# Kernel tuning notes

Hardware: AMD Instinct MI355X
Metric: run time of the kernel (lower is better)

Reference implementation:

```python
import jax, jax.numpy as jnp
import numpy as np

B, S, D = 8, 2048, 768

def setup_inputs():
    key = jax.random.key(0)
    k1, k2, k3, k4 = jax.random.split(key, 4)
    hidden = jax.random.normal(k1, (B, S, D), dtype=jnp.float32)
    # relative lengths in [0.5, 1.0) so every sequence has a realistic valid region
    lengths = 0.5 + 0.5 * jax.random.uniform(k2, (B,), dtype=jnp.float32)
    s = 1.0 / np.sqrt(D)
    W1 = jax.random.uniform(k3, (D, D), minval=-s, maxval=s, dtype=jnp.float32)
    b1 = jnp.zeros((D,), jnp.float32)
    W2 = jax.random.uniform(k4, (D,), minval=-s, maxval=s, dtype=jnp.float32)
    b2 = jnp.zeros((), jnp.float32)
    return {"hidden": hidden, "lengths": lengths, "W1": W1, "b1": b1, "W2": W2, "b2": b2}

def _boundaries(hidden, lengths, W1, b1, W2, b2):
    # Eval-mode boundary prediction (dropout = identity, soft = probs).
    Bn, Sn, _ = hidden.shape
    actual_lens = (lengths * Sn).astype(jnp.int32)                      # [B]
    valid = (jnp.arange(Sn)[None, :] < actual_lens[:, None]).astype(hidden.dtype)  # [B,S]
    h = jax.nn.gelu(hidden @ W1 + b1, approximate=False)                # torch nn.GELU is exact
    logits = h @ W2 + b2                                                # [B,S]
    probs = jax.nn.sigmoid(logits)
    soft = probs * valid
    hard = (probs > 0.5).astype(hidden.dtype) * valid
    last_valid = jnp.clip(actual_lens - 1, 0, Sn - 1)
    bi = jnp.arange(Bn)
    soft = soft.at[bi, last_valid].set(1.0)
    hard = hard.at[bi, last_valid].set(1.0)
    hard_b = hard - jax.lax.stop_gradient(soft) + soft                  # straight-through
    return hard_b, probs * valid, valid, actual_lens

def reference(hidden, lengths, W1, b1, W2, b2):
    Bn, Sn, Dn = hidden.shape
    hard_b, masked_probs, valid, actual_lens = _boundaries(hidden, lengths, W1, b1, W2, b2)
    # K = max segments in the batch (data-dependent -> computed eagerly, as
    # the original torch code does with .item() inside common()).
    K = int(jnp.max(jnp.sum(jax.lax.stop_gradient(hard_b), axis=1)))
    # segment id of each position: boundary token ENDS its segment
    seg_id = jnp.cumsum(hard_b, axis=1) - hard_b                        # [B,S]
    seg_onehot = (jnp.arange(K)[None, None, :]
                  == jax.lax.stop_gradient(seg_id)[:, :, None])          # [B,S,K] == (foo==0)
    segment_mask = seg_onehot.astype(hidden.dtype) * valid[:, :, None]
    counts = jnp.maximum(segment_mask.sum(axis=1), 1.0)                 # [B,K]
    # dense one-hot mask-matmul segment mean, matching the torch bmm formulation
    pooled = jnp.einsum('bsk,bsd->bkd', segment_mask, hidden) / counts[:, :, None]
    nb = (hard_b * valid).sum(axis=1)                                   # boundaries / sample
    max_segments = max(K, 1)
    full = nb >= max_segments - 1
    partial = (nb > 0) & (nb < max_segments - 1)
    shortened = jnp.where(full, 1.0,
                          jnp.where(partial, (nb + 1.0) / max_segments, 0.0))
    return pooled, masked_probs, shortened, nb, actual_lens.astype(jnp.float32)
```

## Files before the change

### kernel.cpp

```cpp
#include <hip/hip_runtime.h>
#include <math.h>

typedef __bf16 bf16x8 __attribute__((ext_vector_type(8)));
typedef float  f32x4  __attribute__((ext_vector_type(4)));

#define NT2 12

__device__ inline float gelu_f(float x) {
    return 0.5f * x * (1.0f + erff(x * 0.70710678118654752f));
}

typedef const __attribute__((address_space(1))) void* gas_t;
typedef __attribute__((address_space(3))) void*       las_t;
__device__ __forceinline__ void gl_lds16(const void* g, void* l) {
    __builtin_amdgcn_global_load_lds((gas_t)g, (las_t)l, 16, 0, 0);
}

__global__ __launch_bounds__(256) void s0_w1t(
    const float* __restrict__ W1, __bf16* __restrict__ Wt, int Dn)
{
    __shared__ float tile[32][33];
    const int k0 = blockIdx.x * 32;
    const int n0 = blockIdx.y * 32;
    const int tx = threadIdx.x & 31, ty = threadIdx.x >> 5;
    #pragma unroll
    for (int p = 0; p < 4; ++p)
        tile[ty + p * 8][tx] = W1[(size_t)(k0 + ty + p * 8) * Dn + n0 + tx];
    __syncthreads();
    #pragma unroll
    for (int p = 0; p < 4; ++p) {
        const int n = n0 + ty + p * 8, k = k0 + tx;
        Wt[(size_t)n * Dn + k] = (__bf16)tile[tx][ty + p * 8];
    }
}

__global__ __launch_bounds__(512) void k1_hyb(
    const float* __restrict__ X, const __bf16* __restrict__ W1t,
    const float* __restrict__ b1, const float* __restrict__ W2,
    float* __restrict__ partial, int Kd)
{
    __shared__ __bf16 Ash[2][128 * 32];
    __shared__ __bf16 Bsh[2][128 * 32];

    const int t    = threadIdx.x;
    const int lane = t & 63;
    const int w    = t >> 6;
    const int wr   = w >> 1;
    const int wc   = w & 1;
    const int ln15 = lane & 15, lg = lane >> 4;
    const int m0   = blockIdx.x * 128;
    const int n0   = blockIdx.y * 128;

    const int ar  = t >> 2, aq = t & 3;
    const int asw = (ar >> 1) & 3;
    const float* gA = X + (size_t)(m0 + ar) * Kd + aq * 8;
    const int    awr = ar * 32 + (aq ^ asw) * 8;

    const int brow = t >> 2;
    const int bkw  = (t & 3) ^ ((brow >> 1) & 3);
    const __bf16* gB = W1t + (size_t)(n0 + brow) * Kd + bkw * 8;

    int aoff[2], boff[4];
    #pragma unroll
    for (int mf = 0; mf < 2; ++mf) {
        const int r = wr * 32 + mf * 16 + ln15;
        aoff[mf] = r * 32 + (lg ^ ((r >> 1) & 3)) * 8;
    }
    #pragma unroll
    for (int nf = 0; nf < 4; ++nf) {
        const int r = wc * 64 + nf * 16 + ln15;
        boff[nf] = r * 32 + (lg ^ ((r >> 1) & 3)) * 8;
    }

    f32x4 acc[2][4];
    #pragma unroll
    for (int i = 0; i < 2; ++i)
        #pragma unroll
        for (int j = 0; j < 4; ++j)
            acc[i][j] = (f32x4){0.f, 0.f, 0.f, 0.f};

    {
        const float4 lo = *(const float4*)(gA);
        const float4 hi = *(const float4*)(gA + 4);
        bf16x8 ab;
        ab[0] = (__bf16)lo.x; ab[1] = (__bf16)lo.y;
        ab[2] = (__bf16)lo.z; ab[3] = (__bf16)lo.w;
        ab[4] = (__bf16)hi.x; ab[5] = (__bf16)hi.y;
        ab[6] = (__bf16)hi.z; ab[7] = (__bf16)hi.w;
        *(bf16x8*)&Ash[0][awr] = ab;
        gl_lds16(gB, &Bsh[0][t * 8]);
    }
    __syncthreads();

    const int nt = Kd / 32;
    int cur = 0;
    for (int kt = 0; kt < nt; ++kt) {
        float4 alo, ahi;
        const bool more = (kt + 1 < nt);
        if (more) {
            const int ko = (kt + 1) * 32;
            alo = *(const float4*)(gA + ko);
            ahi = *(const float4*)(gA + ko + 4);
            gl_lds16(gB + ko, &Bsh[cur ^ 1][t * 8]);
        }

        bf16x8 fa[2], fb[4];
        #pragma unroll
        for (int mf = 0; mf < 2; ++mf)
            fa[mf] = *(const bf16x8*)&Ash[cur][aoff[mf]];
        #pragma unroll
        for (int nf = 0; nf < 4; ++nf)
            fb[nf] = *(const bf16x8*)&Bsh[cur][boff[nf]];
        #pragma unroll
        for (int mf = 0; mf < 2; ++mf)
            #pragma unroll
            for (int nf = 0; nf < 4; ++nf)
                acc[mf][nf] = __builtin_amdgcn_mfma_f32_16x16x32_bf16(
                    fa[mf], fb[nf], acc[mf][nf], 0, 0, 0);

        if (more) {
            bf16x8 ab;
            ab[0] = (__bf16)alo.x; ab[1] = (__bf16)alo.y;
            ab[2] = (__bf16)alo.z; ab[3] = (__bf16)alo.w;
            ab[4] = (__bf16)ahi.x; ab[5] = (__bf16)ahi.y;
            ab[6] = (__bf16)ahi.z; ab[7] = (__bf16)ahi.w;
            *(bf16x8*)&Ash[cur ^ 1][awr] = ab;
        }
        __syncthreads();
        cur ^= 1;
    }

    float b1v[4], w2v[4];
    #pragma unroll
    for (int nf = 0; nf < 4; ++nf) {
        const int n = n0 + wc * 64 + nf * 16 + ln15;
        b1v[nf] = b1[n];
        w2v[nf] = W2[n];
    }
    #pragma unroll
    for (int mf = 0; mf < 2; ++mf)
        #pragma unroll
        for (int j = 0; j < 4; ++j) {
            float s = 0.f;
            #pragma unroll
            for (int nf = 0; nf < 4; ++nf) {
                float c = acc[mf][nf][j] + b1v[nf];
                s += gelu_f(c) * w2v[nf];
            }
            s += __shfl_xor(s, 1);
            s += __shfl_xor(s, 2);
            s += __shfl_xor(s, 4);
            s += __shfl_xor(s, 8);
            if (ln15 == 0) {
                const int m = m0 + wr * 32 + mf * 16 + lg * 4 + j;
                partial[(size_t)m * NT2 + blockIdx.y * 2 + wc] = s;
            }
        }
}

__global__ __launch_bounds__(256) void k2a_logits(
    const float* __restrict__ partial, const float* __restrict__ lengths,
    const float* __restrict__ b2p, float* __restrict__ logits,
    float* __restrict__ out_probs, int S)
{
    const int idx = blockIdx.x * 256 + threadIdx.x;
    const int b = idx / S, s = idx - b * S;
    float sum = b2p[0];
    #pragma unroll
    for (int jt = 0; jt < NT2; ++jt)
        sum += partial[(size_t)idx * NT2 + jt];
    logits[idx] = sum;
    const int len = (int)(lengths[b] * (float)S);
    out_probs[idx] = (s < len) ? 1.0f / (1.0f + expf(-sum)) : 0.0f;
}

__global__ __launch_bounds__(256) void k2b_scan(
    const float* __restrict__ logits, const float* __restrict__ lengths,
    float* __restrict__ out_short, float* __restrict__ out_nb,
    float* __restrict__ out_lens, int* __restrict__ bpos,
    int* __restrict__ nb_arr, int S, int K)
{
    const int b = blockIdx.x;
    const int t = threadIdx.x;
    const int len = (int)(lengths[b] * (float)S);

    __shared__ int cnt[256];
    __shared__ int flags_s[2048];

    const int RP = S / 256;
    const int base_s = t * RP;
    int local = 0;
    #pragma unroll
    for (int r = 0; r < 8; ++r) {
        int s = base_s + r;
        bool v = (s < len);
        int f = (s == len - 1) ? 1 : ((v && logits[(size_t)b * S + s] > 0.0f) ? 1 : 0);
        flags_s[s] = f;
        local += f;
    }
    cnt[t] = local;
    __syncthreads();
    for (int off = 1; off < 256; off <<= 1) {
        int v = cnt[t];
        int u = (t >= off) ? cnt[t - off] : 0;
        __syncthreads();
        cnt[t] = v + u;
        __syncthreads();
    }
    int excl = cnt[t] - local;
    int total = cnt[255];
    for (int r = 0; r < RP; ++r) {
        int s = base_s + r;
        if (flags_s[s]) { bpos[b * S + excl] = s; ++excl; }
    }
    if (t == 0) {
        nb_arr[b] = total;
        float nbf = (float)total;
        float Kf  = (float)K;
        out_nb[b]   = nbf;
        out_lens[b] = (float)len;
        float sh;
        if (nbf >= Kf - 1.0f)      sh = 1.0f;
        else if (nbf > 0.0f)       sh = (nbf + 1.0f) / Kf;
        else                       sh = 0.0f;
        out_short[b] = sh;
    }
}

__global__ __launch_bounds__(192) void k3_pool(
    const float* __restrict__ X, const int* __restrict__ bpos,
    const int* __restrict__ nb_arr, float* __restrict__ pooled,
    int S, int D, int K)
{
    const int bk = blockIdx.x;
    const int b  = bk / K;
    const int k  = bk - b * K;
    const int t  = threadIdx.x;
    const int nb = nb_arr[b];

    float4 acc = {0.f, 0.f, 0.f, 0.f};
    if (k < nb) {
        int start = (k == 0) ? 0 : (bpos[b * S + k - 1] + 1);
        int end   = bpos[b * S + k] + 1;
        float cntf = (float)(end - start);
        for (int s = start; s < end; ++s) {
            const float4 v = *(const float4*)&X[((size_t)b * S + s) * D + t * 4];
            acc.x += v.x; acc.y += v.y; acc.z += v.z; acc.w += v.w;
        }
        acc.x /= cntf; acc.y /= cntf; acc.z /= cntf; acc.w /= cntf;
    }
    *(float4*)&pooled[((size_t)b * K + k) * D + t * 4] = acc;
}

extern "C" void kernel_launch(void* const* d_in, const int* in_sizes, int n_in,
                              void* d_out, int out_size, void* d_ws, size_t ws_size,
                              hipStream_t stream) {
    const float* hidden  = (const float*)d_in[0];
    const float* lengths = (const float*)d_in[1];
    const float* W1      = (const float*)d_in[2];
    const float* b1      = (const float*)d_in[3];
    const float* W2      = (const float*)d_in[4];
    const float* b2      = (const float*)d_in[5];

    const int B = in_sizes[1];
    const int D = in_sizes[3];
    const int S = in_sizes[0] / (B * D);
    const int M = B * S;
    const int K = (out_size - B * S - 3 * B) / (B * D);

    float* out_pooled = (float*)d_out;
    float* out_probs  = out_pooled + (size_t)B * K * D;
    float* out_short  = out_probs + (size_t)B * S;
    float* out_nb     = out_short + B;
    float* out_lens   = out_nb + B;

    char* wsp = (char*)d_ws;
    float* partial = (float*)wsp; wsp += (size_t)M * NT2 * sizeof(float);
    float* logits  = (float*)wsp; wsp += (size_t)M * sizeof(float);
    int*   bpos    = (int*)wsp;   wsp += (size_t)M * sizeof(int);
    int*   nb_arr  = (int*)wsp;

    __bf16* W1t = (__bf16*)out_pooled;

    dim3 gs(D / 32, D / 32);
    s0_w1t<<<gs, 256, 0, stream>>>(W1, W1t, D);

    dim3 g1(M / 128, D / 128);
    k1_hyb<<<g1, 512, 0, stream>>>(hidden, W1t, b1, W2, partial, D);

    k2a_logits<<<M / 256, 256, 0, stream>>>(partial, lengths, b2, logits,
                                            out_probs, S);
    k2b_scan<<<B, 256, 0, stream>>>(logits, lengths, out_short, out_nb,
                                    out_lens, bpos, nb_arr, S, K);
    k3_pool<<<B * K, D / 4, 0, stream>>>(hidden, bpos, nb_arr, out_pooled, S, D, K);
}
```

Measured before the change: 59.11 us.

## Widen GEMM tile to 128x256 with 2x4 warp layout and 1D grid

The fused GEMM+GELU+dot kernel now computes a 128x256 output tile per block instead of 128x128. Each warp covers 64x64 with a 4x4 MFMA fragment grid. The wider tile halves how often the fp32 hidden activations are re-read and converted to bf16 across N-tiles, and it raises MFMA work per LDS fragment load. The grid becomes 1D with consecutive blocks sharing the same row tile, which may improve L2 reuse of X. The cost is twice the accumulator registers and more LDS per block, which may lower occupancy, and fewer blocks (384), which may underfill the CUs.

```diff
diff --git a/kernel.cpp b/kernel.cpp
--- a/kernel.cpp
+++ b/kernel.cpp
@@ -34,36 +34,40 @@
     }
 }
 
-__global__ __launch_bounds__(512) void k1_hyb(
+__global__ __launch_bounds__(512) void k1_wide(
     const float* __restrict__ X, const __bf16* __restrict__ W1t,
     const float* __restrict__ b1, const float* __restrict__ W2,
-    float* __restrict__ partial, int Kd)
+    float* __restrict__ partial, int Kd, int ny)
 {
     __shared__ __bf16 Ash[2][128 * 32];
-    __shared__ __bf16 Bsh[2][128 * 32];
+    __shared__ __bf16 Bsh[2][256 * 32];
+
+    const int bid = blockIdx.x;
+    const int bx  = bid / ny;
+    const int by  = bid - bx * ny;
 
     const int t    = threadIdx.x;
     const int lane = t & 63;
     const int w    = t >> 6;
-    const int wr   = w >> 1;
-    const int wc   = w & 1;
+    const int wr   = w >> 2;
+    const int wc   = w & 3;
     const int ln15 = lane & 15, lg = lane >> 4;
-    const int m0   = blockIdx.x * 128;
-    const int n0   = blockIdx.y * 128;
+    const int m0   = bx * 128;
+    const int n0   = by * 256;
 
     const int ar  = t >> 2, aq = t & 3;
-    const int asw = (ar >> 1) & 3;
     const float* gA = X + (size_t)(m0 + ar) * Kd + aq * 8;
-    const int    awr = ar * 32 + (aq ^ asw) * 8;
-
-    const int brow = t >> 2;
-    const int bkw  = (t & 3) ^ ((brow >> 1) & 3);
-    const __bf16* gB = W1t + (size_t)(n0 + brow) * Kd + bkw * 8;
-
-    int aoff[2], boff[4];
-    #pragma unroll
-    for (int mf = 0; mf < 2; ++mf) {
-        const int r = wr * 32 + mf * 16 + ln15;
+    const int    awr = ar * 32 + (aq ^ ((ar >> 1) & 3)) * 8;
+
+    const int br0 = t >> 2,        bq0 = (t & 3) ^ ((br0 >> 1) & 3);
+    const int br1 = (t >> 2) + 128, bq1 = (t & 3) ^ ((br1 >> 1) & 3);
+    const __bf16* gB0 = W1t + (size_t)(n0 + br0) * Kd + bq0 * 8;
+    const __bf16* gB1 = W1t + (size_t)(n0 + br1) * Kd + bq1 * 8;
+
+    int aoff[4], boff[4];
+    #pragma unroll
+    for (int mf = 0; mf < 4; ++mf) {
+        const int r = wr * 64 + mf * 16 + ln15;
         aoff[mf] = r * 32 + (lg ^ ((r >> 1) & 3)) * 8;
     }
     #pragma unroll
@@ -72,9 +76,9 @@
         boff[nf] = r * 32 + (lg ^ ((r >> 1) & 3)) * 8;
     }
 
-    f32x4 acc[2][4];
-    #pragma unroll
-    for (int i = 0; i < 2; ++i)
+    f32x4 acc[4][4];
+    #pragma unroll
+    for (int i = 0; i < 4; ++i)
         #pragma unroll
         for (int j = 0; j < 4; ++j)
             acc[i][j] = (f32x4){0.f, 0.f, 0.f, 0.f};
@@ -88,7 +92,8 @@
         ab[4] = (__bf16)hi.x; ab[5] = (__bf16)hi.y;
         ab[6] = (__bf16)hi.z; ab[7] = (__bf16)hi.w;
         *(bf16x8*)&Ash[0][awr] = ab;
-        gl_lds16(gB, &Bsh[0][t * 8]);
+        gl_lds16(gB0, &Bsh[0][t * 8]);
+        gl_lds16(gB1, &Bsh[0][(t + 512) * 8]);
     }
     __syncthreads();
 
@@ -101,18 +106,19 @@
             const int ko = (kt + 1) * 32;
             alo = *(const float4*)(gA + ko);
             ahi = *(const float4*)(gA + ko + 4);
-            gl_lds16(gB + ko, &Bsh[cur ^ 1][t * 8]);
+            gl_lds16(gB0 + ko, &Bsh[cur ^ 1][t * 8]);
+            gl_lds16(gB1 + ko, &Bsh[cur ^ 1][(t + 512) * 8]);
         }
 
-        bf16x8 fa[2], fb[4];
-        #pragma unroll
-        for (int mf = 0; mf < 2; ++mf)
+        bf16x8 fa[4], fb[4];
+        #pragma unroll
+        for (int mf = 0; mf < 4; ++mf)
             fa[mf] = *(const bf16x8*)&Ash[cur][aoff[mf]];
         #pragma unroll
         for (int nf = 0; nf < 4; ++nf)
             fb[nf] = *(const bf16x8*)&Bsh[cur][boff[nf]];
         #pragma unroll
-        for (int mf = 0; mf < 2; ++mf)
+        for (int mf = 0; mf < 4; ++mf)
             #pragma unroll
             for (int nf = 0; nf < 4; ++nf)
                 acc[mf][nf] = __builtin_amdgcn_mfma_f32_16x16x32_bf16(
@@ -138,7 +144,7 @@
         w2v[nf] = W2[n];
     }
     #pragma unroll
-    for (int mf = 0; mf < 2; ++mf)
+    for (int mf = 0; mf < 4; ++mf)
         #pragma unroll
         for (int j = 0; j < 4; ++j) {
             float s = 0.f;
@@ -152,8 +158,8 @@
             s += __shfl_xor(s, 4);
             s += __shfl_xor(s, 8);
             if (ln15 == 0) {
-                const int m = m0 + wr * 32 + mf * 16 + lg * 4 + j;
-                partial[(size_t)m * NT2 + blockIdx.y * 2 + wc] = s;
+                const int m = m0 + wr * 64 + mf * 16 + lg * 4 + j;
+                partial[(size_t)m * NT2 + by * 4 + wc] = s;
             }
         }
 }
@@ -285,8 +291,8 @@
     dim3 gs(D / 32, D / 32);
     s0_w1t<<<gs, 256, 0, stream>>>(W1, W1t, D);
 
-    dim3 g1(M / 128, D / 128);
-    k1_hyb<<<g1, 512, 0, stream>>>(hidden, W1t, b1, W2, partial, D);
+    const int nx = M / 128, ny = D / 256;
+    k1_wide<<<nx * ny, 512, 0, stream>>>(hidden, W1t, b1, W2, partial, D, ny);
 
     k2a_logits<<<M / 256, 256, 0, stream>>>(partial, lengths, b2, logits,
                                             out_probs, S);
```

New measurement: 69.74 us. 1.18x slower.

## Compute full hidden width per block so each input row is read once

Applied to the files above, without the earlier changes.

The first-layer GEMM kernel now gives each block 64 rows and all 768 output columns, instead of a 128x128 tile on a 2D grid. Each row of the fp32 hidden input is then loaded and converted to bf16 only once rather than once per column tile, which cuts global memory traffic for the largest operand. The cost is a large double-buffered LDS footprint for the whole transposed weight slice and 96 accumulator registers per thread. That limits the GPU to roughly one block per CU and gives a grid of only 256 blocks, so there is less latency hiding.

```diff
diff --git a/kernel.cpp b/kernel.cpp
--- a/kernel.cpp
+++ b/kernel.cpp
@@ -2,6 +2,7 @@
 #include <math.h>
 
 typedef __bf16 bf16x8 __attribute__((ext_vector_type(8)));
+typedef __bf16 bf16x4 __attribute__((ext_vector_type(4)));
 typedef float  f32x4  __attribute__((ext_vector_type(4)));
 
 #define NT2 12
@@ -34,128 +35,137 @@
     }
 }
 
-__global__ __launch_bounds__(512) void k1_hyb(
+__global__ __launch_bounds__(512) void k1_row(
     const float* __restrict__ X, const __bf16* __restrict__ W1t,
     const float* __restrict__ b1, const float* __restrict__ W2,
     float* __restrict__ partial, int Kd)
 {
-    __shared__ __bf16 Ash[2][128 * 32];
-    __shared__ __bf16 Bsh[2][128 * 32];
+    __shared__ __bf16 Ash[2][64 * 32];
+    __shared__ __bf16 Bsh[2][768 * 32];
 
     const int t    = threadIdx.x;
     const int lane = t & 63;
     const int w    = t >> 6;
-    const int wr   = w >> 1;
-    const int wc   = w & 1;
+    const int wr   = w >> 2;
+    const int wc   = w & 3;
     const int ln15 = lane & 15, lg = lane >> 4;
-    const int m0   = blockIdx.x * 128;
-    const int n0   = blockIdx.y * 128;
-
-    const int ar  = t >> 2, aq = t & 3;
-    const int asw = (ar >> 1) & 3;
-    const float* gA = X + (size_t)(m0 + ar) * Kd + aq * 8;
-    const int    awr = ar * 32 + (aq ^ asw) * 8;
-
-    const int brow = t >> 2;
-    const int bkw  = (t & 3) ^ ((brow >> 1) & 3);
-    const __bf16* gB = W1t + (size_t)(n0 + brow) * Kd + bkw * 8;
-
-    int aoff[2], boff[4];
+    const int m0   = blockIdx.x * 64;
+
+    const int ar = t >> 3, ag = t & 7;
+    const float* gA = X + (size_t)(m0 + ar) * Kd + ag * 4;
+    const int awr = ar * 32 + (ag ^ ((((ar >> 1) & 3)) << 1)) * 4;
+
+    const int br  = t >> 2;
+    const int bkw = (t & 3) ^ ((br >> 1) & 3);
+    const __bf16* gBbase = W1t + (size_t)br * Kd + bkw * 8;
+
+    int aoff[2], boff[3][4];
     #pragma unroll
     for (int mf = 0; mf < 2; ++mf) {
         const int r = wr * 32 + mf * 16 + ln15;
         aoff[mf] = r * 32 + (lg ^ ((r >> 1) & 3)) * 8;
     }
     #pragma unroll
-    for (int nf = 0; nf < 4; ++nf) {
-        const int r = wc * 64 + nf * 16 + ln15;
-        boff[nf] = r * 32 + (lg ^ ((r >> 1) & 3)) * 8;
-    }
-
-    f32x4 acc[2][4];
-    #pragma unroll
-    for (int i = 0; i < 2; ++i)
-        #pragma unroll
-        for (int j = 0; j < 4; ++j)
-            acc[i][j] = (f32x4){0.f, 0.f, 0.f, 0.f};
+    for (int rep = 0; rep < 3; ++rep)
+        #pragma unroll
+        for (int nf = 0; nf < 4; ++nf) {
+            const int rb = (wc + 4 * rep) * 64 + nf * 16 + ln15;
+            boff[rep][nf] = rb * 32 + (lg ^ ((rb >> 1) & 3)) * 8;
+        }
+
+    f32x4 acc[3][2][4];
+    #pragma unroll
+    for (int rep = 0; rep < 3; ++rep)
+        #pragma unroll
+        for (int i = 0; i < 2; ++i)
+            #pragma unroll
+            for (int j = 0; j < 4; ++j)
+                acc[rep][i][j] = (f32x4){0.f, 0.f, 0.f, 0.f};
 
     {
-        const float4 lo = *(const float4*)(gA);
-        const float4 hi = *(const float4*)(gA + 4);
-        bf16x8 ab;
-        ab[0] = (__bf16)lo.x; ab[1] = (__bf16)lo.y;
-        ab[2] = (__bf16)lo.z; ab[3] = (__bf16)lo.w;
-        ab[4] = (__bf16)hi.x; ab[5] = (__bf16)hi.y;
-        ab[6] = (__bf16)hi.z; ab[7] = (__bf16)hi.w;
-        *(bf16x8*)&Ash[0][awr] = ab;
-        gl_lds16(gB, &Bsh[0][t * 8]);
+        const float4 a4 = *(const float4*)(gA);
+        bf16x4 ab;
+        ab[0] = (__bf16)a4.x; ab[1] = (__bf16)a4.y;
+        ab[2] = (__bf16)a4.z; ab[3] = (__bf16)a4.w;
+        *(bf16x4*)&Ash[0][awr] = ab;
+        #pragma unroll
+        for (int i = 0; i < 6; ++i)
+            gl_lds16(gBbase + (size_t)128 * i * Kd, &Bsh[0][(t + 512 * i) * 8]);
     }
     __syncthreads();
 
     const int nt = Kd / 32;
     int cur = 0;
     for (int kt = 0; kt < nt; ++kt) {
-        float4 alo, ahi;
+        float4 a4;
         const bool more = (kt + 1 < nt);
         if (more) {
             const int ko = (kt + 1) * 32;
-            alo = *(const float4*)(gA + ko);
-            ahi = *(const float4*)(gA + ko + 4);
-            gl_lds16(gB + ko, &Bsh[cur ^ 1][t * 8]);
-        }
-
-        bf16x8 fa[2], fb[4];
+            a4 = *(const float4*)(gA + ko);
+            #pragma unroll
+            for (int i = 0; i < 6; ++i)
+                gl_lds16(gBbase + (size_t)128 * i * Kd + ko,
+                         &Bsh[cur ^ 1][(t + 512 * i) * 8]);
+        }
+
+        bf16x8 fa[2];
         #pragma unroll
         for (int mf = 0; mf < 2; ++mf)
             fa[mf] = *(const bf16x8*)&Ash[cur][aoff[mf]];
         #pragma unroll
-        for (int nf = 0; nf < 4; ++nf)
-            fb[nf] = *(const bf16x8*)&Bsh[cur][boff[nf]];
-        #pragma unroll
-        for (int mf = 0; mf < 2; ++mf)
+        for (int rep = 0; rep < 3; ++rep) {
+            bf16x8 fb[4];
             #pragma unroll
             for (int nf = 0; nf < 4; ++nf)
-                acc[mf][nf] = __builtin_amdgcn_mfma_f32_16x16x32_bf16(
-                    fa[mf], fb[nf], acc[mf][nf], 0, 0, 0);
+                fb[nf] = *(const bf16x8*)&Bsh[cur][boff[rep][nf]];
+            #pragma unroll
+            for (int mf = 0; mf < 2; ++mf)
+                #pragma unroll
+                for (int nf = 0; nf < 4; ++nf)
+                    acc[rep][mf][nf] = __builtin_amdgcn_mfma_f32_16x16x32_bf16(
+                        fa[mf], fb[nf], acc[rep][mf][nf], 0, 0, 0);
+        }
 
         if (more) {
-            bf16x8 ab;
-            ab[0] = (__bf16)alo.x; ab[1] = (__bf16)alo.y;
-            ab[2] = (__bf16)alo.z; ab[3] = (__bf16)alo.w;
-            ab[4] = (__bf16)ahi.x; ab[5] = (__bf16)ahi.y;
-            ab[6] = (__bf16)ahi.z; ab[7] = (__bf16)ahi.w;
-            *(bf16x8*)&Ash[cur ^ 1][awr] = ab;
+            bf16x4 ab;
+            ab[0] = (__bf16)a4.x; ab[1] = (__bf16)a4.y;
+            ab[2] = (__bf16)a4.z; ab[3] = (__bf16)a4.w;
+            *(bf16x4*)&Ash[cur ^ 1][awr] = ab;
         }
         __syncthreads();
         cur ^= 1;
     }
 
-    float b1v[4], w2v[4];
-    #pragma unroll
-    for (int nf = 0; nf < 4; ++nf) {
-        const int n = n0 + wc * 64 + nf * 16 + ln15;
-        b1v[nf] = b1[n];
-        w2v[nf] = W2[n];
-    }
-    #pragma unroll
-    for (int mf = 0; mf < 2; ++mf)
-        #pragma unroll
-        for (int j = 0; j < 4; ++j) {
-            float s = 0.f;
-            #pragma unroll
-            for (int nf = 0; nf < 4; ++nf) {
-                float c = acc[mf][nf][j] + b1v[nf];
-                s += gelu_f(c) * w2v[nf];
+    #pragma unroll
+    for (int rep = 0; rep < 3; ++rep) {
+        const int slot = wc + 4 * rep;
+        float b1v[4], w2v[4];
+        #pragma unroll
+        for (int nf = 0; nf < 4; ++nf) {
+            const int n = slot * 64 + nf * 16 + ln15;
+            b1v[nf] = b1[n];
+            w2v[nf] = W2[n];
+        }
+        #pragma unroll
+        for (int mf = 0; mf < 2; ++mf)
+            #pragma unroll
+            for (int j = 0; j < 4; ++j) {
+                float s = 0.f;
+                #pragma unroll
+                for (int nf = 0; nf < 4; ++nf) {
+                    float c = acc[rep][mf][nf][j] + b1v[nf];
+                    s += gelu_f(c) * w2v[nf];
+                }
+                s += __shfl_xor(s, 1);
+                s += __shfl_xor(s, 2);
+                s += __shfl_xor(s, 4);
+                s += __shfl_xor(s, 8);
+                if (ln15 == 0) {
+                    const int m = m0 + wr * 32 + mf * 16 + lg * 4 + j;
+                    partial[(size_t)m * NT2 + slot] = s;
+                }
             }
-            s += __shfl_xor(s, 1);
-            s += __shfl_xor(s, 2);
-            s += __shfl_xor(s, 4);
-            s += __shfl_xor(s, 8);
-            if (ln15 == 0) {
-                const int m = m0 + wr * 32 + mf * 16 + lg * 4 + j;
-                partial[(size_t)m * NT2 + blockIdx.y * 2 + wc] = s;
-            }
-        }
+    }
 }
 
 __global__ __launch_bounds__(256) void k2a_logits(
@@ -285,8 +295,7 @@
     dim3 gs(D / 32, D / 32);
     s0_w1t<<<gs, 256, 0, stream>>>(W1, W1t, D);
 
-    dim3 g1(M / 128, D / 128);
-    k1_hyb<<<g1, 512, 0, stream>>>(hidden, W1t, b1, W2, partial, D);
+    k1_row<<<M / 64, 512, 0, stream>>>(hidden, W1t, b1, W2, partial, D);
 
     k2a_logits<<<M / 256, 256, 0, stream>>>(partial, lengths, b2, logits,
                                             out_probs, S);
```

Result: slower. 79.45 us (+34.4%).
